# Kernel tuning notes

Measured on AMD Instinct MI355X. Metric: run time of the kernel, lower is better.

Reference implementation:

```python
import jax, jax.numpy as jnp
import numpy as np
import math

B, T, C, H = 2, 2048, 512, 8
K, DIL = 3, 1
EPS = 1e-5


def _ln(x, g, b):
    m = jnp.mean(x, axis=-1, keepdims=True)
    v = jnp.mean(jnp.square(x - m), axis=-1, keepdims=True)
    return (x - m) * jax.lax.rsqrt(v + EPS) * g + b


def setup_inputs() -> dict:
    key = jax.random.key(0)
    ks = jax.random.split(key, 12)
    s = 0.02
    return {
        "x": jax.random.normal(ks[0], (B, T, C), jnp.float32),
        "conv_w": jax.random.normal(ks[1], (C, C, K), jnp.float32) * s,  # OIH
        "conv_b": jax.random.normal(ks[2], (C,), jnp.float32) * s,
        "g1": jnp.ones((C,), jnp.float32), "b1": jnp.zeros((C,), jnp.float32),
        "qkv_w": jax.random.normal(ks[3], (C, 3 * C), jnp.float32) * s,
        "qkv_b": jax.random.normal(ks[4], (3 * C,), jnp.float32) * s,
        "proj_w": jax.random.normal(ks[5], (C, C), jnp.float32) * s,
        "proj_b": jax.random.normal(ks[6], (C,), jnp.float32) * s,
        "g2": jnp.ones((C,), jnp.float32), "b2": jnp.zeros((C,), jnp.float32),
        "ffn_w1": jax.random.normal(ks[7], (C, 2 * C), jnp.float32) * s,
        "ffn_b1": jax.random.normal(ks[8], (2 * C,), jnp.float32) * s,
        "ffn_w2": jax.random.normal(ks[9], (2 * C, C), jnp.float32) * s,
        "ffn_b2": jax.random.normal(ks[10], (C,), jnp.float32) * s,
        "g3": jnp.ones((C,), jnp.float32), "b3": jnp.zeros((C,), jnp.float32),
    }


def reference(x, conv_w, conv_b, g1, b1, qkv_w, qkv_b, proj_w, proj_b,
              g2, b2, ffn_w1, ffn_b1, ffn_w2, ffn_b2, g3, b3):
    b, t, c = x.shape
    hd = c // H
    # --- causal dilated conv (left-pad only == pad both + right-trim) ---
    pad = (K - 1) * DIL
    xc = jnp.transpose(x, (0, 2, 1))  # [B,C,T]
    conv = jax.lax.conv_general_dilated(
        xc, conv_w, window_strides=(1,), padding=[(pad, 0)],
        rhs_dilation=(DIL,), dimension_numbers=("NCH", "OIH", "NCH"))
    conv = conv + conv_b[None, :, None]
    x = _ln(x + jnp.transpose(conv, (0, 2, 1)), g1, b1)
    # --- causal self-attention ---
    qkv = (x @ qkv_w + qkv_b).reshape(b, t, 3, H, hd)
    qkv = jnp.transpose(qkv, (2, 0, 3, 1, 4))  # [3,B,H,T,hd]
    q, k, v = qkv[0], qkv[1], qkv[2]
    scores = jnp.einsum("bhqd,bhkd->bhqk", q, k) / math.sqrt(hd)
    causal = jnp.tril(jnp.ones((t, t), bool))
    scores = jnp.where(causal, scores, -jnp.inf)
    attn = jax.nn.softmax(scores, axis=-1)
    out = jnp.einsum("bhqk,bhkd->bhqd", attn, v)
    out = jnp.transpose(out, (0, 2, 1, 3)).reshape(b, t, c)
    out = out @ proj_w + proj_b
    x = _ln(x + out, g2, b2)
    # --- FFN ---
    ffn = jax.nn.relu(x @ ffn_w1 + ffn_b1) @ ffn_w2 + ffn_b2
    return _ln(x + ffn, g3, b3)
```

## Files before the change

### kernel.cpp

```cpp
#include <hip/hip_runtime.h>
#include <hip/hip_bf16.h>

#define TT 2048
#define QSC 0.18033688011112042f

typedef __attribute__((ext_vector_type(4))) float f32x4;
typedef __attribute__((ext_vector_type(8))) __bf16 bf16x8;
typedef __attribute__((ext_vector_type(4))) short short4v;
typedef __attribute__((ext_vector_type(8))) short short8v;

enum { M_CONV = 0, M_QKV = 1, M_PROJ = 2, M_FFN1 = 3, M_FFN2 = 4 };

__device__ __forceinline__ void gload16(const void* g, void* l) {
    __builtin_amdgcn_global_load_lds(
        (__attribute__((address_space(1))) void*)g,
        (__attribute__((address_space(3))) void*)l, 16, 0, 0);
}

__device__ __forceinline__ short f2bf(float f) {
    unsigned u = __float_as_uint(f);
    u = (u + 0x7fffu + ((u >> 16) & 1u)) >> 16;
    return (short)u;
}

__device__ __forceinline__ float bf2f(short s) {
    unsigned u = ((unsigned)(unsigned short)s) << 16;
    return __uint_as_float(u);
}

__global__ __launch_bounds__(256) void prep_all(
    const float* __restrict__ conv_w, const float* __restrict__ x,
    const float* __restrict__ qkv_w, const float* __restrict__ proj_w,
    const float* __restrict__ f1w, const float* __restrict__ f2w,
    short* __restrict__ cwT, short* __restrict__ xpad,
    short* __restrict__ qkvT, short* __restrict__ projT,
    short* __restrict__ f1T, short* __restrict__ f2T) {
    if (blockIdx.x < 2048) {
        int t = blockIdx.x;
        const float* src; short* dst; int K, N, lt;
        if (t < 768)       { src = qkv_w;  dst = qkvT;  K = 512;  N = 1536; lt = t; }
        else if (t < 1024) { src = proj_w; dst = projT; K = 512;  N = 512;  lt = t - 768; }
        else if (t < 1536) { src = f1w;    dst = f1T;   K = 512;  N = 1024; lt = t - 1024; }
        else               { src = f2w;    dst = f2T;   K = 1024; N = 512;  lt = t - 1536; }
        int ntn = N >> 5;
        int kt = lt / ntn, nt = lt - kt * ntn;
        int k0 = kt * 32, n0 = nt * 32;
        __shared__ float tile[32][33];
        int c = threadIdx.x & 31, r = threadIdx.x >> 5;
        #pragma unroll
        for (int i = 0; i < 4; i++)
            tile[r + i * 8][c] = src[(size_t)(k0 + r + i * 8) * N + n0 + c];
        __syncthreads();
        #pragma unroll
        for (int i = 0; i < 4; i++)
            dst[(size_t)(n0 + r + i * 8) * K + k0 + c] = f2bf(tile[c][r + i * 8]);
        return;
    }
    if (blockIdx.x < 3072) {
        int oi = (blockIdx.x - 2048) * 256 + threadIdx.x;
        int o = oi >> 9, i = oi & 511;
        const float* s = conv_w + (size_t)oi * 3;
        #pragma unroll
        for (int tap = 0; tap < 3; tap++)
            cwT[(size_t)o * 1536 + tap * 512 + i] = f2bf(s[tap]);
        return;
    }
    int idx = (blockIdx.x - 3072) * 256 + threadIdx.x;
    int rp = idx >> 6, j = idx & 63;
    if (rp < 4100) {
        int bb = rp / 2050, rr = rp - bb * 2050;
        int t = rr - 2;
        short8v pk;
        if (t >= 0) {
            const float* xs = x + ((size_t)(bb << 11) + t) * 512 + j * 8;
            f32x4 a = *(const f32x4*)xs;
            f32x4 b2 = *(const f32x4*)(xs + 4);
            #pragma unroll
            for (int i = 0; i < 4; i++) { pk[i] = f2bf(a[i]); pk[i + 4] = f2bf(b2[i]); }
        } else {
            #pragma unroll
            for (int i = 0; i < 8; i++) pk[i] = 0;
        }
        *(short8v*)&xpad[(size_t)rp * 512 + j * 8] = pk;
    }
}

__global__ __launch_bounds__(512) void ln_row(const short* __restrict__ in,
                                              const float* __restrict__ g,
                                              const float* __restrict__ b,
                                              float* __restrict__ outf,
                                              short* __restrict__ outb) {
    int row = blockIdx.x * 8 + (threadIdx.x >> 6);
    int l = threadIdx.x & 63;
    short8v v = *(const short8v*)(in + (size_t)row * 512 + l * 8);
    float vf[8];
    float s = 0.f, ss = 0.f;
    #pragma unroll
    for (int i = 0; i < 8; i++) {
        vf[i] = bf2f(v[i]);
        s += vf[i]; ss += vf[i] * vf[i];
    }
    #pragma unroll
    for (int off = 1; off < 64; off <<= 1) {
        s  += __shfl_xor(s, off);
        ss += __shfl_xor(ss, off);
    }
    float mean = s * (1.f / 512);
    float var  = ss * (1.f / 512) - mean * mean;
    float rstd = rsqrtf(var + 1e-5f);
    f32x4 g0 = *(const f32x4*)(g + l * 8), g1 = *(const f32x4*)(g + l * 8 + 4);
    f32x4 b0 = *(const f32x4*)(b + l * 8), b1 = *(const f32x4*)(b + l * 8 + 4);
    float ov[8];
    #pragma unroll
    for (int i = 0; i < 4; i++) {
        ov[i]     = (vf[i]     - mean) * rstd * g0[i] + b0[i];
        ov[i + 4] = (vf[i + 4] - mean) * rstd * g1[i] + b1[i];
    }
    if (outf) {
        float* q = outf + (size_t)row * 512 + l * 8;
        *(f32x4*)q       = (f32x4){ov[0], ov[1], ov[2], ov[3]};
        *(f32x4*)(q + 4) = (f32x4){ov[4], ov[5], ov[6], ov[7]};
    }
    if (outb) {
        short8v pk;
        #pragma unroll
        for (int i = 0; i < 8; i++) pk[i] = f2bf(ov[i]);
        *(short8v*)(outb + (size_t)row * 512 + l * 8) = pk;
    }
}

template<int MODE>
__device__ __forceinline__ const short* a_ptr(const short* A, int m0, int r, int kk, int K) {
    if constexpr (MODE == M_CONV) {
        int row = m0 + r;
        int bb = row >> 11, t5 = row & 2047;
        int tap = kk >> 9, k2 = kk & 511;
        return A + ((size_t)(bb * 2050 + t5 + tap) * 512 + k2);
    } else {
        return A + ((size_t)(m0 + r) * K + kk);
    }
}

template<int MODE, int BM, int BN>
__global__ __launch_bounds__((BM == 64) ? 128 : 256) void gemm_mfma(
    const short* __restrict__ A, const short* __restrict__ Bw,
    const float* __restrict__ bias, const void* __restrict__ res,
    void* __restrict__ Cout, short* __restrict__ vTb, int K) {
    constexpr int NT  = (BM == 64) ? 128 : 256;
    constexpr int MF  = (BM == 64) ? 2 : 4;
    constexpr int NF  = 2;
    constexpr int ACH = (BM * 64 * 2) / (16 * NT);
    constexpr int BCH = (BN * 64 * 2) / (16 * NT);
    __shared__ short As[BM * 64];
    __shared__ short Bs[BN * 64];
    const int tid = threadIdx.x;
    const int w = tid >> 6, l = tid & 63;
    const int lr = l & 15, lc = l >> 4;
    const int wrb = (BM == 64) ? (w * 32) : ((w >> 1) * 64);
    const int wcb = (BM == 64) ? 0 : ((w & 1) * 32);
    const int m0 = blockIdx.x * BM, n0 = blockIdx.y * BN;
    f32x4 acc[MF][NF];
    #pragma unroll
    for (int mf = 0; mf < MF; mf++)
        #pragma unroll
        for (int nf = 0; nf < NF; nf++) acc[mf][nf] = (f32x4){0.f, 0.f, 0.f, 0.f};

    for (int k0 = 0; k0 < K; k0 += 64) {
        #pragma unroll
        for (int i = 0; i < ACH; i++) {
            int u = i * NT + tid, r = u >> 3, c = (u & 7) ^ (r & 7);
            gload16(a_ptr<MODE>(A, m0, r, k0 + c * 8, K), (char*)As + u * 16);
        }
        #pragma unroll
        for (int i = 0; i < BCH; i++) {
            int u = i * NT + tid, r = u >> 3, c = (u & 7) ^ (r & 7);
            gload16(Bw + ((size_t)(n0 + r) * K + k0 + c * 8), (char*)Bs + u * 16);
        }
        __syncthreads();
        bf16x8 af[MF][2], bfv[NF][2];
        #pragma unroll
        for (int mf = 0; mf < MF; mf++)
            #pragma unroll
            for (int ks = 0; ks < 2; ks++) {
                int rr = wrb + mf * 16 + lr;
                int cc = (ks * 4 + lc) ^ (rr & 7);
                af[mf][ks] = *(const bf16x8*)&As[rr * 64 + cc * 8];
            }
        #pragma unroll
        for (int nf = 0; nf < NF; nf++)
            #pragma unroll
            for (int ks = 0; ks < 2; ks++) {
                int rr = wcb + nf * 16 + lr;
                int cc = (ks * 4 + lc) ^ (rr & 7);
                bfv[nf][ks] = *(const bf16x8*)&Bs[rr * 64 + cc * 8];
            }
        __builtin_amdgcn_s_setprio(1);
        #pragma unroll
        for (int nf = 0; nf < NF; nf++)
            #pragma unroll
            for (int ks = 0; ks < 2; ks++)
                #pragma unroll
                for (int mf = 0; mf < MF; mf++)
                    acc[mf][nf] = __builtin_amdgcn_mfma_f32_16x16x32_bf16(
                        af[mf][ks], bfv[nf][ks], acc[mf][nf], 0, 0, 0);
        __builtin_amdgcn_s_setprio(0);
        __syncthreads();
    }
    #pragma unroll
    for (int mf = 0; mf < MF; mf++) {
        int row0 = m0 + wrb + mf * 16 + lc * 4;
        #pragma unroll
        for (int nf = 0; nf < NF; nf++) {
            int col = n0 + wcb + nf * 16 + lr;
            float bv = bias[col];
            if constexpr (MODE == M_CONV) {
                short* Cb = (short*)Cout;
                const float* rf = (const float*)res;
                #pragma unroll
                for (int rg = 0; rg < 4; rg++) {
                    size_t off = (size_t)(row0 + rg) * 512 + col;
                    Cb[off] = f2bf(acc[mf][nf][rg] + bv + rf[off]);
                }
            } else if constexpr (MODE == M_PROJ || MODE == M_FFN2) {
                short* Cb = (short*)Cout;
                const short* rb = (const short*)res;
                #pragma unroll
                for (int rg = 0; rg < 4; rg++) {
                    size_t off = (size_t)(row0 + rg) * 512 + col;
                    Cb[off] = f2bf(acc[mf][nf][rg] + bv + bf2f(rb[off]));
                }
            } else if constexpr (MODE == M_FFN1) {
                short* Cb = (short*)Cout;
                #pragma unroll
                for (int rg = 0; rg < 4; rg++)
                    Cb[(size_t)(row0 + rg) * 1024 + col] =
                        f2bf(fmaxf(acc[mf][nf][rg] + bv, 0.f));
            } else {
                short* Cb = (short*)Cout;
                float v[4];
                #pragma unroll
                for (int rg = 0; rg < 4; rg++) {
                    v[rg] = acc[mf][nf][rg] + bv;
                    float wv = (col < 512) ? v[rg] * QSC : v[rg];
                    Cb[(size_t)(row0 + rg) * 1536 + col] = f2bf(wv);
                }
                if (col >= 1024) {
                    int vc = col - 1024, hh = vc >> 6, dd = vc & 63;
                    int bb = row0 >> 11, t5 = row0 & 2047;
                    short4v pk = {f2bf(v[0]), f2bf(v[1]), f2bf(v[2]), f2bf(v[3])};
                    *(short4v*)&vTb[((size_t)((bb << 3) + hh) * 64 + dd) * 2048 + t5] = pk;
                }
            }
        }
    }
}

__global__ __launch_bounds__(256) void attn_part(const short* __restrict__ qkvb,
                                                 const short* __restrict__ vTb,
                                                 short* __restrict__ pO,
                                                 float* __restrict__ pML) {
    __shared__ short SM[20992];
    __bf16* SMb = (__bf16*)SM;
    const int tid = threadIdx.x;
    const int w = tid >> 6, l = tid & 63;
    const int lr = l & 15, lc = l >> 4;
    const int L = blockIdx.x;
    const int bh = L & 15;
    const int par = (L >> 4) & 3;
    const int qt = 31 - (L >> 6);
    const int b = bh >> 3, h = bh & 7;
    const int qr = w * 16, q0 = qt * 64;
    const int pbase = 16384 + w * (16 * 72);
    const int ntiles = (qt >= par) ? ((qt - par) >> 2) + 1 : 0;

    #pragma unroll
    for (int i = 0; i < 2; i++) {
        int u = i * 256 + tid, r = u >> 3, c = (u & 7) ^ (r & 7);
        gload16(qkvb + ((size_t)(b * 2048 + q0 + r) * 1536 + h * 64 + c * 8),
                (char*)&SM[16384] + u * 16);
        if (ntiles > 0) {
            gload16(qkvb + ((size_t)(b * 2048 + par * 64 + r) * 1536 + 512 + h * 64 + c * 8),
                    (char*)&SM[0] + u * 16);
            gload16(vTb + ((size_t)(bh * 64 + r) * 2048 + par * 64 + c * 8),
                    (char*)&SM[8192] + u * 16);
        }
    }
    __syncthreads();
    bf16x8 aq[2];
    #pragma unroll
    for (int ks = 0; ks < 2; ks++) {
        int rr = qr + lr;
        int cc = (lc + 4 * ks) ^ (rr & 7);
        aq[ks] = *(const bf16x8*)&SM[16384 + rr * 64 + cc * 8];
    }
    __syncthreads();

    bf16x8 onesf;
    #pragma unroll
    for (int i = 0; i < 8; i++) onesf[i] = (__bf16)1.0f;

    f32x4 o[4], lacc;
    float mst[4];
    #pragma unroll
    for (int nf = 0; nf < 4; nf++) o[nf] = (f32x4){0.f, 0.f, 0.f, 0.f};
    lacc = (f32x4){0.f, 0.f, 0.f, 0.f};
    #pragma unroll
    for (int rg = 0; rg < 4; rg++) mst[rg] = -1e30f;

    for (int s = 0; s < ntiles; s++) {
        const int kt = par + 4 * s;
        const int cur = s & 1;
        if (s + 1 < ntiles) {
            int ktn = kt + 4, nb = (cur ^ 1) * 4096;
            #pragma unroll
            for (int i = 0; i < 2; i++) {
                int u = i * 256 + tid, r = u >> 3, c = (u & 7) ^ (r & 7);
                gload16(qkvb + ((size_t)(b * 2048 + ktn * 64 + r) * 1536 + 512 + h * 64 + c * 8),
                        (char*)&SM[nb] + u * 16);
                gload16(vTb + ((size_t)(bh * 64 + r) * 2048 + ktn * 64 + c * 8),
                        (char*)&SM[8192 + nb] + u * 16);
            }
        }
        f32x4 s4[4];
        #pragma unroll
        for (int nf = 0; nf < 4; nf++) s4[nf] = (f32x4){0.f, 0.f, 0.f, 0.f};
        __builtin_amdgcn_s_setprio(1);
        #pragma unroll
        for (int nf = 0; nf < 4; nf++) {
            #pragma unroll
            for (int ks = 0; ks < 2; ks++) {
                int rr = nf * 16 + lr;
                int cc = (lc + 4 * ks) ^ (rr & 7);
                bf16x8 bk = *(const bf16x8*)&SM[cur * 4096 + rr * 64 + cc * 8];
                s4[nf] = __builtin_amdgcn_mfma_f32_16x16x32_bf16(aq[ks], bk, s4[nf], 0, 0, 0);
            }
        }
        __builtin_amdgcn_s_setprio(0);
        const bool diag = (kt == qt);
        if (diag) {
            #pragma unroll
            for (int nf = 0; nf < 4; nf++)
                #pragma unroll
                for (int rg = 0; rg < 4; rg++)
                    if (nf * 16 + lr > qr + lc * 4 + rg) s4[nf][rg] = -1e30f;
        }
        float rm[4];
        int ok = 1;
        #pragma unroll
        for (int rg = 0; rg < 4; rg++) {
            float m_ = fmaxf(fmaxf(s4[0][rg], s4[1][rg]), fmaxf(s4[2][rg], s4[3][rg]));
            m_ = fmaxf(m_, __shfl_xor(m_, 1));
            m_ = fmaxf(m_, __shfl_xor(m_, 2));
            m_ = fmaxf(m_, __shfl_xor(m_, 4));
            m_ = fmaxf(m_, __shfl_xor(m_, 8));
            rm[rg] = m_;
            ok &= (m_ <= mst[rg] + 11.5f);
        }
        if (!__all(ok)) {
            #pragma unroll
            for (int rg = 0; rg < 4; rg++) {
                float mn = fmaxf(mst[rg], rm[rg]);
                float alpha = exp2f(mst[rg] - mn);
                mst[rg] = mn;
                lacc[rg] *= alpha;
                #pragma unroll
                for (int nf = 0; nf < 4; nf++) o[nf][rg] *= alpha;
            }
        }
        #pragma unroll
        for (int rg = 0; rg < 4; rg++) {
            int prow = pbase + (lc * 4 + rg) * 72;
            SMb[prow      + lr] = (__bf16)exp2f(s4[0][rg] - mst[rg]);
            SMb[prow + 16 + lr] = (__bf16)exp2f(s4[1][rg] - mst[rg]);
            SMb[prow + 32 + lr] = (__bf16)exp2f(s4[2][rg] - mst[rg]);
            SMb[prow + 48 + lr] = (__bf16)exp2f(s4[3][rg] - mst[rg]);
        }
        bf16x8 pa[2];
        #pragma unroll
        for (int ks = 0; ks < 2; ks++)
            pa[ks] = *(const bf16x8*)&SM[pbase + lr * 72 + ks * 32 + lc * 8];
        __builtin_amdgcn_s_setprio(1);
        #pragma unroll
        for (int ks = 0; ks < 2; ks++)
            lacc = __builtin_amdgcn_mfma_f32_16x16x32_bf16(pa[ks], onesf, lacc, 0, 0, 0);
        #pragma unroll
        for (int nf = 0; nf < 4; nf++) {
            #pragma unroll
            for (int ks = 0; ks < 2; ks++) {
                int rr = nf * 16 + lr;
                int cc = (lc + 4 * ks) ^ (rr & 7);
                bf16x8 bv = *(const bf16x8*)&SM[8192 + cur * 4096 + rr * 64 + cc * 8];
                o[nf] = __builtin_amdgcn_mfma_f32_16x16x32_bf16(pa[ks], bv, o[nf], 0, 0, 0);
            }
        }
        __builtin_amdgcn_s_setprio(0);
        __syncthreads();
    }

    size_t ob = (size_t)L * 4096;
    #pragma unroll
    for (int nf = 0; nf < 4; nf++) {
        #pragma unroll
        for (int rg = 0; rg < 4; rg++) {
            int rw = qr + lc * 4 + rg;
            pO[ob + rw * 64 + nf * 16 + lr] = (ntiles > 0) ? f2bf(o[nf][rg]) : (short)0;
        }
    }
    if (lr == 0) {
        #pragma unroll
        for (int rg = 0; rg < 4; rg++) {
            int rw = qr + lc * 4 + rg;
            pML[(size_t)L * 128 + rw]      = (ntiles > 0) ? mst[rg] : -1e30f;
            pML[(size_t)L * 128 + 64 + rw] = (ntiles > 0) ? lacc[rg] : 0.f;
        }
    }
}

__global__ __launch_bounds__(256) void attn_merge(const short* __restrict__ pO,
                                                  const float* __restrict__ pML,
                                                  short* __restrict__ aout) {
    int U = blockIdx.x;
    int bh = U & 15, qt = U >> 4;
    int b = bh >> 3, h = bh & 7, q0 = qt * 64;
    int Lb = ((31 - qt) << 6) | bh;
    int t = threadIdx.x;
    int r = t >> 2, cs = (t & 3) * 16;
    float m[4], lv[4];
    #pragma unroll
    for (int pp = 0; pp < 4; pp++) {
        m[pp]  = pML[(size_t)(Lb | (pp << 4)) * 128 + r];
        lv[pp] = pML[(size_t)(Lb | (pp << 4)) * 128 + 64 + r];
    }
    float mn = fmaxf(fmaxf(m[0], m[1]), fmaxf(m[2], m[3]));
    float a[4], den = 0.f;
    #pragma unroll
    for (int pp = 0; pp < 4; pp++) { a[pp] = exp2f(m[pp] - mn); den += lv[pp] * a[pp]; }
    float inv = 1.f / den;
    #pragma unroll
    for (int half = 0; half < 2; half++) {
        int c0 = cs + half * 8;
        float accv[8];
        #pragma unroll
        for (int j = 0; j < 8; j++) accv[j] = 0.f;
        #pragma unroll
        for (int pp = 0; pp < 4; pp++) {
            short8v ov = *(const short8v*)&pO[(size_t)(Lb | (pp << 4)) * 4096 + r * 64 + c0];
            #pragma unroll
            for (int j = 0; j < 8; j++) accv[j] += bf2f(ov[j]) * a[pp];
        }
        short8v res;
        #pragma unroll
        for (int j = 0; j < 8; j++) res[j] = f2bf(accv[j] * inv);
        *(short8v*)&aout[(size_t)(b * 2048 + q0 + r) * 512 + h * 64 + c0] = res;
    }
}

extern "C" void kernel_launch(void* const* d_in, const int* in_sizes, int n_in,
                              void* d_out, int out_size, void* d_ws, size_t ws_size,
                              hipStream_t stream) {
    const float* x      = (const float*)d_in[0];
    const float* conv_w = (const float*)d_in[1];
    const float* conv_b = (const float*)d_in[2];
    const float* g1     = (const float*)d_in[3];
    const float* b1     = (const float*)d_in[4];
    const float* qkv_w  = (const float*)d_in[5];
    const float* qkv_b  = (const float*)d_in[6];
    const float* proj_w = (const float*)d_in[7];
    const float* proj_b = (const float*)d_in[8];
    const float* g2     = (const float*)d_in[9];
    const float* b2     = (const float*)d_in[10];
    const float* ffn_w1 = (const float*)d_in[11];
    const float* ffn_b1 = (const float*)d_in[12];
    const float* ffn_w2 = (const float*)d_in[13];
    const float* ffn_b2 = (const float*)d_in[14];
    const float* g3     = (const float*)d_in[15];
    const float* b3     = (const float*)d_in[16];
    float* out = (float*)d_out;

    char* p = (char*)d_ws;
    short* cwT   = (short*)p;  p += 786432 * 2;
    short* qkvT  = (short*)p;  p += 786432 * 2;
    short* projT = (short*)p;  p += 262144 * 2;
    short* f1T   = (short*)p;  p += 524288 * 2;
    short* f2T   = (short*)p;  p += 524288 * 2;
    short* xpad  = (short*)p;  p += 2099200 * 2;
    short* yb    = (short*)p;  p += 2097152 * 2;
    short* x1b   = (short*)p;  p += 2097152 * 2;
    short* qkvb  = (short*)p;  p += 6291456 * 2;
    short* vTb   = (short*)p;  p += 2097152 * 2;
    short* pO    = (short*)p;  p += 8388608 * 2;
    float* pML   = (float*)p;  p += 262144 * 4;
    short* x2b     = x1b;
    short* hb      = qkvb;
    short* attnout = xpad;

    prep_all<<<4097, 256, 0, stream>>>(conv_w, x, qkv_w, proj_w, ffn_w1, ffn_w2,
                                       cwT, xpad, qkvT, projT, f1T, f2T);
    gemm_mfma<M_CONV, 64, 32><<<dim3(64, 16), 128, 0, stream>>>(
        xpad, cwT, conv_b, x, yb, nullptr, 1536);
    ln_row<<<512, 512, 0, stream>>>(yb, g1, b1, nullptr, x1b);
    gemm_mfma<M_QKV, 128, 64><<<dim3(32, 24), 256, 0, stream>>>(
        x1b, qkvT, qkv_b, nullptr, qkvb, vTb, 512);
    attn_part<<<2048, 256, 0, stream>>>(qkvb, vTb, pO, pML);
    attn_merge<<<512, 256, 0, stream>>>(pO, pML, attnout);
    gemm_mfma<M_PROJ, 64, 32><<<dim3(64, 16), 128, 0, stream>>>(
        attnout, projT, proj_b, x1b, yb, nullptr, 512);
    ln_row<<<512, 512, 0, stream>>>(yb, g2, b2, nullptr, x2b);
    gemm_mfma<M_FFN1, 128, 64><<<dim3(32, 16), 256, 0, stream>>>(
        x2b, f1T, ffn_b1, nullptr, hb, nullptr, 512);
    gemm_mfma<M_FFN2, 64, 32><<<dim3(64, 16), 128, 0, stream>>>(
        hb, f2T, ffn_b2, x2b, yb, nullptr, 1024);
    ln_row<<<512, 512, 0, stream>>>(yb, g3, b3, out, nullptr);
}
```

Baseline: 119.4 us.

## Process 128 query rows per attention block to reuse K/V tiles

```diff
diff --git a/kernel.cpp b/kernel.cpp
--- a/kernel.cpp
+++ b/kernel.cpp
@@ -267,18 +267,34 @@
     const int L = blockIdx.x;
     const int bh = L & 15;
     const int par = (L >> 4) & 3;
-    const int qt = 31 - (L >> 6);
+    const int qh = 15 - (L >> 6);
     const int b = bh >> 3, h = bh & 7;
-    const int qr = w * 16, q0 = qt * 64;
+    const int q0 = qh * 128;
     const int pbase = 16384 + w * (16 * 72);
-    const int ntiles = (qt >= par) ? ((qt - par) >> 2) + 1 : 0;
-
-    #pragma unroll
-    for (int i = 0; i < 2; i++) {
+    const int top = 2 * qh + 1;
+    const int ntiles = (top >= par) ? ((top - par) >> 2) + 1 : 0;
+
+    #pragma unroll
+    for (int i = 0; i < 4; i++) {
         int u = i * 256 + tid, r = u >> 3, c = (u & 7) ^ (r & 7);
         gload16(qkvb + ((size_t)(b * 2048 + q0 + r) * 1536 + h * 64 + c * 8),
-                (char*)&SM[16384] + u * 16);
-        if (ntiles > 0) {
+                (char*)&SM[0] + u * 16);
+    }
+    __syncthreads();
+    bf16x8 aq[2][2];
+    #pragma unroll
+    for (int mf = 0; mf < 2; mf++)
+        #pragma unroll
+        for (int ks = 0; ks < 2; ks++) {
+            int rr = w * 32 + mf * 16 + lr;
+            int cc = (lc + 4 * ks) ^ (rr & 7);
+            aq[mf][ks] = *(const bf16x8*)&SM[rr * 64 + cc * 8];
+        }
+    __syncthreads();
+    if (ntiles > 0) {
+        #pragma unroll
+        for (int i = 0; i < 2; i++) {
+            int u = i * 256 + tid, r = u >> 3, c = (u & 7) ^ (r & 7);
             gload16(qkvb + ((size_t)(b * 2048 + par * 64 + r) * 1536 + 512 + h * 64 + c * 8),
                     (char*)&SM[0] + u * 16);
             gload16(vTb + ((size_t)(bh * 64 + r) * 2048 + par * 64 + c * 8),
@@ -286,26 +302,21 @@
         }
     }
     __syncthreads();
-    bf16x8 aq[2];
-    #pragma unroll
-    for (int ks = 0; ks < 2; ks++) {
-        int rr = qr + lr;
-        int cc = (lc + 4 * ks) ^ (rr & 7);
-        aq[ks] = *(const bf16x8*)&SM[16384 + rr * 64 + cc * 8];
-    }
-    __syncthreads();
 
     bf16x8 onesf;
     #pragma unroll
     for (int i = 0; i < 8; i++) onesf[i] = (__bf16)1.0f;
 
-    f32x4 o[4], lacc;
-    float mst[4];
-    #pragma unroll
-    for (int nf = 0; nf < 4; nf++) o[nf] = (f32x4){0.f, 0.f, 0.f, 0.f};
-    lacc = (f32x4){0.f, 0.f, 0.f, 0.f};
-    #pragma unroll
-    for (int rg = 0; rg < 4; rg++) mst[rg] = -1e30f;
+    f32x4 o[2][4], lacc[2];
+    float mst[2][4];
+    #pragma unroll
+    for (int mf = 0; mf < 2; mf++) {
+        lacc[mf] = (f32x4){0.f, 0.f, 0.f, 0.f};
+        #pragma unroll
+        for (int nf = 0; nf < 4; nf++) o[mf][nf] = (f32x4){0.f, 0.f, 0.f, 0.f};
+        #pragma unroll
+        for (int rg = 0; rg < 4; rg++) mst[mf][rg] = -1e30f;
+    }
 
     for (int s = 0; s < ntiles; s++) {
         const int kt = par + 4 * s;
@@ -321,97 +332,106 @@
                         (char*)&SM[8192 + nb] + u * 16);
             }
         }
-        f32x4 s4[4];
-        #pragma unroll
-        for (int nf = 0; nf < 4; nf++) s4[nf] = (f32x4){0.f, 0.f, 0.f, 0.f};
-        __builtin_amdgcn_s_setprio(1);
+        const bool crossing = (kt >= 2 * qh);
+        #pragma unroll
+        for (int mf = 0; mf < 2; mf++) {
+            f32x4 s4[4];
+            #pragma unroll
+            for (int nf = 0; nf < 4; nf++) s4[nf] = (f32x4){0.f, 0.f, 0.f, 0.f};
+            __builtin_amdgcn_s_setprio(1);
+            #pragma unroll
+            for (int nf = 0; nf < 4; nf++) {
+                #pragma unroll
+                for (int ks = 0; ks < 2; ks++) {
+                    int rr = nf * 16 + lr;
+                    int cc = (lc + 4 * ks) ^ (rr & 7);
+                    bf16x8 bk = *(const bf16x8*)&SM[cur * 4096 + rr * 64 + cc * 8];
+                    s4[nf] = __builtin_amdgcn_mfma_f32_16x16x32_bf16(aq[mf][ks], bk, s4[nf], 0, 0, 0);
+                }
+            }
+            __builtin_amdgcn_s_setprio(0);
+            if (crossing) {
+                int rowb = q0 + w * 32 + mf * 16 + lc * 4;
+                #pragma unroll
+                for (int nf = 0; nf < 4; nf++) {
+                    int colg = kt * 64 + nf * 16 + lr;
+                    #pragma unroll
+                    for (int rg = 0; rg < 4; rg++)
+                        if (colg > rowb + rg) s4[nf][rg] = -1e30f;
+                }
+            }
+            float rm[4];
+            int ok = 1;
+            #pragma unroll
+            for (int rg = 0; rg < 4; rg++) {
+                float m_ = fmaxf(fmaxf(s4[0][rg], s4[1][rg]), fmaxf(s4[2][rg], s4[3][rg]));
+                m_ = fmaxf(m_, __shfl_xor(m_, 1));
+                m_ = fmaxf(m_, __shfl_xor(m_, 2));
+                m_ = fmaxf(m_, __shfl_xor(m_, 4));
+                m_ = fmaxf(m_, __shfl_xor(m_, 8));
+                rm[rg] = m_;
+                ok &= (m_ <= mst[mf][rg] + 11.5f);
+            }
+            if (!__all(ok)) {
+                #pragma unroll
+                for (int rg = 0; rg < 4; rg++) {
+                    float mn = fmaxf(mst[mf][rg], rm[rg]);
+                    float alpha = exp2f(mst[mf][rg] - mn);
+                    mst[mf][rg] = mn;
+                    lacc[mf][rg] *= alpha;
+                    #pragma unroll
+                    for (int nf = 0; nf < 4; nf++) o[mf][nf][rg] *= alpha;
+                }
+            }
+            #pragma unroll
+            for (int rg = 0; rg < 4; rg++) {
+                int prow = pbase + (lc * 4 + rg) * 72;
+                SMb[prow      + lr] = (__bf16)exp2f(s4[0][rg] - mst[mf][rg]);
+                SMb[prow + 16 + lr] = (__bf16)exp2f(s4[1][rg] - mst[mf][rg]);
+                SMb[prow + 32 + lr] = (__bf16)exp2f(s4[2][rg] - mst[mf][rg]);
+                SMb[prow + 48 + lr] = (__bf16)exp2f(s4[3][rg] - mst[mf][rg]);
+            }
+            bf16x8 pa[2];
+            #pragma unroll
+            for (int ks = 0; ks < 2; ks++)
+                pa[ks] = *(const bf16x8*)&SM[pbase + lr * 72 + ks * 32 + lc * 8];
+            __builtin_amdgcn_s_setprio(1);
+            #pragma unroll
+            for (int ks = 0; ks < 2; ks++)
+                lacc[mf] = __builtin_amdgcn_mfma_f32_16x16x32_bf16(pa[ks], onesf, lacc[mf], 0, 0, 0);
+            #pragma unroll
+            for (int nf = 0; nf < 4; nf++) {
+                #pragma unroll
+                for (int ks = 0; ks < 2; ks++) {
+                    int rr = nf * 16 + lr;
+                    int cc = (lc + 4 * ks) ^ (rr & 7);
+                    bf16x8 bv = *(const bf16x8*)&SM[8192 + cur * 4096 + rr * 64 + cc * 8];
+                    o[mf][nf] = __builtin_amdgcn_mfma_f32_16x16x32_bf16(pa[ks], bv, o[mf][nf], 0, 0, 0);
+                }
+            }
+            __builtin_amdgcn_s_setprio(0);
+        }
+        __syncthreads();
+    }
+
+    size_t ob = (size_t)L * 8192;
+    #pragma unroll
+    for (int mf = 0; mf < 2; mf++) {
         #pragma unroll
         for (int nf = 0; nf < 4; nf++) {
             #pragma unroll
-            for (int ks = 0; ks < 2; ks++) {
-                int rr = nf * 16 + lr;
-                int cc = (lc + 4 * ks) ^ (rr & 7);
-                bf16x8 bk = *(const bf16x8*)&SM[cur * 4096 + rr * 64 + cc * 8];
-                s4[nf] = __builtin_amdgcn_mfma_f32_16x16x32_bf16(aq[ks], bk, s4[nf], 0, 0, 0);
-            }
-        }
-        __builtin_amdgcn_s_setprio(0);
-        const bool diag = (kt == qt);
-        if (diag) {
-            #pragma unroll
-            for (int nf = 0; nf < 4; nf++)
-                #pragma unroll
-                for (int rg = 0; rg < 4; rg++)
-                    if (nf * 16 + lr > qr + lc * 4 + rg) s4[nf][rg] = -1e30f;
-        }
-        float rm[4];
-        int ok = 1;
-        #pragma unroll
-        for (int rg = 0; rg < 4; rg++) {
-            float m_ = fmaxf(fmaxf(s4[0][rg], s4[1][rg]), fmaxf(s4[2][rg], s4[3][rg]));
-            m_ = fmaxf(m_, __shfl_xor(m_, 1));
-            m_ = fmaxf(m_, __shfl_xor(m_, 2));
-            m_ = fmaxf(m_, __shfl_xor(m_, 4));
-            m_ = fmaxf(m_, __shfl_xor(m_, 8));
-            rm[rg] = m_;
-            ok &= (m_ <= mst[rg] + 11.5f);
-        }
-        if (!__all(ok)) {
-            #pragma unroll
             for (int rg = 0; rg < 4; rg++) {
-                float mn = fmaxf(mst[rg], rm[rg]);
-                float alpha = exp2f(mst[rg] - mn);
-                mst[rg] = mn;
-                lacc[rg] *= alpha;
-                #pragma unroll
-                for (int nf = 0; nf < 4; nf++) o[nf][rg] *= alpha;
-            }
-        }
-        #pragma unroll
-        for (int rg = 0; rg < 4; rg++) {
-            int prow = pbase + (lc * 4 + rg) * 72;
-            SMb[prow      + lr] = (__bf16)exp2f(s4[0][rg] - mst[rg]);
-            SMb[prow + 16 + lr] = (__bf16)exp2f(s4[1][rg] - mst[rg]);
-            SMb[prow + 32 + lr] = (__bf16)exp2f(s4[2][rg] - mst[rg]);
-            SMb[prow + 48 + lr] = (__bf16)exp2f(s4[3][rg] - mst[rg]);
-        }
-        bf16x8 pa[2];
-        #pragma unroll
-        for (int ks = 0; ks < 2; ks++)
-            pa[ks] = *(const bf16x8*)&SM[pbase + lr * 72 + ks * 32 + lc * 8];
-        __builtin_amdgcn_s_setprio(1);
-        #pragma unroll
-        for (int ks = 0; ks < 2; ks++)
-            lacc = __builtin_amdgcn_mfma_f32_16x16x32_bf16(pa[ks], onesf, lacc, 0, 0, 0);
-        #pragma unroll
-        for (int nf = 0; nf < 4; nf++) {
-            #pragma unroll
-            for (int ks = 0; ks < 2; ks++) {
-                int rr = nf * 16 + lr;
-                int cc = (lc + 4 * ks) ^ (rr & 7);
-                bf16x8 bv = *(const bf16x8*)&SM[8192 + cur * 4096 + rr * 64 + cc * 8];
-                o[nf] = __builtin_amdgcn_mfma_f32_16x16x32_bf16(pa[ks], bv, o[nf], 0, 0, 0);
-            }
-        }
-        __builtin_amdgcn_s_setprio(0);
-        __syncthreads();
-    }
-
-    size_t ob = (size_t)L * 4096;
-    #pragma unroll
-    for (int nf = 0; nf < 4; nf++) {
-        #pragma unroll
-        for (int rg = 0; rg < 4; rg++) {
-            int rw = qr + lc * 4 + rg;
-            pO[ob + rw * 64 + nf * 16 + lr] = (ntiles > 0) ? f2bf(o[nf][rg]) : (short)0;
-        }
-    }
-    if (lr == 0) {
-        #pragma unroll
-        for (int rg = 0; rg < 4; rg++) {
-            int rw = qr + lc * 4 + rg;
-            pML[(size_t)L * 128 + rw]      = (ntiles > 0) ? mst[rg] : -1e30f;
-            pML[(size_t)L * 128 + 64 + rw] = (ntiles > 0) ? lacc[rg] : 0.f;
+                int rw = w * 32 + mf * 16 + lc * 4 + rg;
+                pO[ob + rw * 64 + nf * 16 + lr] = f2bf(o[mf][nf][rg]);
+            }
+        }
+        if (lr == 0) {
+            #pragma unroll
+            for (int rg = 0; rg < 4; rg++) {
+                int rw = w * 32 + mf * 16 + lc * 4 + rg;
+                pML[(size_t)L * 256 + rw]       = mst[mf][rg];
+                pML[(size_t)L * 256 + 128 + rw] = lacc[mf][rg];
+            }
         }
     }
 }
@@ -422,14 +442,16 @@
     int U = blockIdx.x;
     int bh = U & 15, qt = U >> 4;
     int b = bh >> 3, h = bh & 7, q0 = qt * 64;
-    int Lb = ((31 - qt) << 6) | bh;
+    int qh = qt >> 1, rowofs = (qt & 1) * 64;
+    int Lb = ((15 - qh) << 6) | bh;
     int t = threadIdx.x;
     int r = t >> 2, cs = (t & 3) * 16;
+    int rr = rowofs + r;
     float m[4], lv[4];
     #pragma unroll
     for (int pp = 0; pp < 4; pp++) {
-        m[pp]  = pML[(size_t)(Lb | (pp << 4)) * 128 + r];
-        lv[pp] = pML[(size_t)(Lb | (pp << 4)) * 128 + 64 + r];
+        m[pp]  = pML[(size_t)(Lb | (pp << 4)) * 256 + rr];
+        lv[pp] = pML[(size_t)(Lb | (pp << 4)) * 256 + 128 + rr];
     }
     float mn = fmaxf(fmaxf(m[0], m[1]), fmaxf(m[2], m[3]));
     float a[4], den = 0.f;
@@ -444,7 +466,7 @@
         for (int j = 0; j < 8; j++) accv[j] = 0.f;
         #pragma unroll
         for (int pp = 0; pp < 4; pp++) {
-            short8v ov = *(const short8v*)&pO[(size_t)(Lb | (pp << 4)) * 4096 + r * 64 + c0];
+            short8v ov = *(const short8v*)&pO[(size_t)(Lb | (pp << 4)) * 8192 + rr * 64 + c0];
             #pragma unroll
             for (int j = 0; j < 8; j++) accv[j] += bf2f(ov[j]) * a[pp];
         }
@@ -501,7 +523,7 @@
     ln_row<<<512, 512, 0, stream>>>(yb, g1, b1, nullptr, x1b);
     gemm_mfma<M_QKV, 128, 64><<<dim3(32, 24), 256, 0, stream>>>(
         x1b, qkvT, qkv_b, nullptr, qkvb, vTb, 512);
-    attn_part<<<2048, 256, 0, stream>>>(qkvb, vTb, pO, pML);
+    attn_part<<<1024, 256, 0, stream>>>(qkvb, vTb, pO, pML);
     attn_merge<<<512, 256, 0, stream>>>(pO, pML, attnout);
     gemm_mfma<M_PROJ, 64, 32><<<dim3(64, 16), 128, 0, stream>>>(
         attnout, projT, proj_b, x1b, yb, nullptr, 512);
```

Result: slower. 123.3 us (+3.3%).
